# Kernel tuning notes

Hardware: AMD Instinct MI355X
Metric: run time of the kernel (lower is better)

The kernel has to match this reference:

```python
import jax, jax.numpy as jnp
import numpy as np

DT = 0.1       # integration step (ms)
TAU_M = 10.0   # membrane time constant
TAU_S = 5.0    # synaptic time constant
E_REV = 1.0    # synaptic reversal potential
G_MAX = 1.0    # synaptic conductance scale
P, N, E, B, T = 8, 2048, 16, 4, 128


def setup_inputs() -> dict:
    key = jax.random.key(0)
    k_src, k_tgt, k_w, k_win = jax.random.split(key, 4)
    t_seq = jnp.arange(B * T, dtype=jnp.float32).reshape(B, T) * DT  # [B,T] times in ms
    src = jax.random.randint(k_src, (E,), 0, P, dtype=jnp.int32)
    tgt = jax.random.randint(k_tgt, (E,), 0, P, dtype=jnp.int32)
    W = jax.random.normal(k_w, (E, N, N), jnp.float32) * (1.0 / np.sqrt(N))
    W_in = jax.random.normal(k_win, (N, N), jnp.float32) * (1.0 / np.sqrt(N))
    v0 = jnp.zeros((P, B, N), jnp.float32)      # population states
    s0 = jnp.zeros((E, B, N), jnp.float32)      # recurrent synapse states
    s_in0 = jnp.zeros((B, N), jnp.float32)      # input synapse state
    return dict(t_seq=t_seq, W=W, W_in=W_in, v0=v0, s0=s0, s_in0=s_in0, src=src, tgt=tgt)


def _input_rate(t, n):
    # InputPopulation: firing rate is a pure function of time t, per-unit phase.
    phase = jnp.arange(n, dtype=jnp.float32) * (2.0 * jnp.pi / n)
    return 0.5 * (1.0 + jnp.sin(2.0 * jnp.pi * t[:, None] / 100.0 + phase[None, :]))  # [B,n]


def _simulate(t_seq, W, W_in, v0, s0, s_in0, src, tgt):
    n_pop = v0.shape[0]

    def step(carry, t):  # t: [B] current time
        v, s, s_in, err = carry
        rates = jax.nn.sigmoid(v)                      # [P,B,N] firing rates
        # --- synapse message passing: gather pre rates, dense projection ---
        pre = rates[src]                               # [E,B,N]
        drive = jnp.einsum('ebi,eij->ebj', pre, W)     # [E,B,N]
        s_new = s + DT * (-s / TAU_S + drive)          # exponential synapse state
        # --- input population synapse (pre rate is a function of t) ---
        rate_in = _input_rate(t, v.shape[-1])          # [B,N]
        s_in_new = s_in + DT * (-s_in / TAU_S + rate_in @ W_in)
        # --- conductance-based currents scattered into target populations ---
        post_v = v[tgt]                                # [E,B,N]
        I_e = G_MAX * s_new * (E_REV - post_v)
        g_e = G_MAX * s_new
        I_sum = jax.ops.segment_sum(I_e, tgt, num_segments=n_pop)  # [P,B,N]
        g_sum = jax.ops.segment_sum(g_e, tgt, num_segments=n_pop)
        I_in = G_MAX * s_in_new * (E_REV - v[0])
        I_sum = I_sum.at[0].add(I_in)
        g_sum = g_sum.at[0].add(G_MAX * s_in_new)
        # --- Euler integrator step + stability error accumulation ---
        dv = (-v - g_sum * v + I_sum) / TAU_M
        v_new = v + DT * dv
        err_new = err + jnp.mean(jnp.abs(dv)) * DT
        return (v_new, s_new, s_in_new, err_new), jax.nn.sigmoid(v_new)

    init = (v0, s0, s_in0, jnp.zeros((), jnp.float32))
    (v_f, s_f, s_in_f, err), rates_seq = jax.lax.scan(step, init, t_seq.T)  # rates_seq: [T,P,B,N]
    firing_rates = jnp.transpose(rates_seq, (2, 0, 1, 3))  # [B,T,P,N]
    return firing_rates, err


def reference(t_seq, W, W_in, v0, s0, s_in0, src, tgt):
    return _simulate(t_seq, W, W_in, v0, s0, s_in0, src, tgt)
```

## Files before the change

### kernel.cpp

```cpp
#include <hip/hip_runtime.h>
#include <hip/hip_bf16.h>
#include <math.h>

#define DT_     0.1f
#define TAU_M_  10.0f
#define TAU_S_  5.0f
#define NP_     8
#define NN_     2048
#define NE_     16
#define NB_     4
#define NT_     128

#define CH_     32
#define IL_     64
#define NEDGE_  17

typedef __attribute__((ext_vector_type(8))) _Float16 half8;
typedef __attribute__((ext_vector_type(8))) float    float8;

template <typename T> struct V8;
template <> struct V8<float>    { typedef float8 type; };
template <> struct V8<_Float16> { typedef half8  type; };

__device__ __forceinline__ float sigmoidf_(float x) {
  return 1.0f / (1.0f + expf(-x));
}

__global__ __launch_bounds__(256) void k_convert(
    const float* __restrict__ W, const float* __restrict__ W_in,
    _Float16* __restrict__ Wh) {
  size_t idx = ((size_t)blockIdx.x * 256 + threadIdx.x) * 8;
  const size_t lim = (size_t)NE_ * NN_ * NN_;
  const float* src = (idx < lim) ? (W + idx) : (W_in + (idx - lim));
  float4 a = *(const float4*)src;
  float4 b = *(const float4*)(src + 4);
  half8 h;
  h[0] = (_Float16)a.x; h[1] = (_Float16)a.y; h[2] = (_Float16)a.z; h[3] = (_Float16)a.w;
  h[4] = (_Float16)b.x; h[5] = (_Float16)b.y; h[6] = (_Float16)b.z; h[7] = (_Float16)b.w;
  *(half8*)(Wh + idx) = h;
}

__global__ __launch_bounds__(256) void k_init(
    const float* __restrict__ v0, const float* __restrict__ s0,
    const float* __restrict__ s_in0,
    float* __restrict__ v, float* __restrict__ s, float* __restrict__ s_in,
    float* __restrict__ rates, float* __restrict__ errpart) {
  int idx = blockIdx.x * 256 + threadIdx.x;
  if (idx < NE_ * NB_ * NN_) s[idx] = s0[idx];
  if (idx < NP_ * NB_ * NN_) {
    float vv = v0[idx];
    v[idx] = vv;
    rates[idx] = sigmoidf_(vv);
  }
  if (idx < NB_ * NN_) s_in[idx] = s_in0[idx];
  if (idx < 256) errpart[idx] = 0.0f;
}

template <typename WT>
__global__ __launch_bounds__(256) void k_stepA(
    const WT* __restrict__ Wall, const WT* __restrict__ Win,
    const float* __restrict__ rates, const float* __restrict__ t_seq,
    const int* __restrict__ src, _Float16* __restrict__ part, int step) {
  const int e   = blockIdx.x;
  const int ch  = blockIdx.y;
  const int tid = threadIdx.x;

  __shared__ float pre[NB_][IL_];
  const int i0 = ch * IL_;

  if (tid < NB_ * IL_) {
    int b  = tid >> 6;
    int il = tid & (IL_ - 1);
    float val;
    if (e == 16) {
      float t = t_seq[b * NT_ + step];
      float phase = (float)(i0 + il) * (6.2831853071795864f / (float)NN_);
      val = 0.5f * (1.0f + sinf(0.062831853071795864f * t + phase));
    } else {
      val = rates[(src[e] * NB_ + b) * NN_ + (i0 + il)];
    }
    pre[b][il] = val;
  }
  __syncthreads();

  const WT* Wp = (e == 16) ? Win : (Wall + (size_t)e * NN_ * NN_);
  const int j = tid * 8;

  float acc[NB_][8] = {};
  typedef typename V8<WT>::type vec8;
#pragma unroll 8
  for (int il = 0; il < IL_; ++il) {
    vec8 w = *(const vec8*)(Wp + (size_t)(i0 + il) * NN_ + j);
    float wf[8];
#pragma unroll
    for (int k = 0; k < 8; ++k) wf[k] = (float)w[k];
#pragma unroll
    for (int b = 0; b < NB_; ++b) {
      float p = pre[b][il];
#pragma unroll
      for (int k = 0; k < 8; ++k) acc[b][k] += p * wf[k];
    }
  }

#pragma unroll
  for (int b = 0; b < NB_; ++b) {
    half8 o;
#pragma unroll
    for (int k = 0; k < 8; ++k) o[k] = (_Float16)acc[b][k];
    *(half8*)(part + (((size_t)ch * NEDGE_ + e) * NB_ + b) * NN_ + j) = o;
  }
}

__global__ __launch_bounds__(256) void k_stepR(
    const _Float16* __restrict__ part, float* __restrict__ s,
    float* __restrict__ s_in) {
  const int idx = blockIdx.x * 256 + threadIdx.x;
  const int e  = idx >> 10;
  const int r  = idx & 1023;
  const int b  = r >> 8;
  const int n  = (r & 255) * 8;

  float acc[8] = {};
#pragma unroll
  for (int c = 0; c < CH_; ++c) {
    half8 pv = *(const half8*)(part + (((size_t)c * NEDGE_ + e) * NB_ + b) * NN_ + n);
#pragma unroll
    for (int k = 0; k < 8; ++k) acc[k] += (float)pv[k];
  }

  float* sp = (e == 16) ? (s_in + b * NN_ + n) : (s + ((size_t)e * NB_ + b) * NN_ + n);
  float4 s0 = *(const float4*)sp;
  float4 s1 = *(const float4*)(sp + 4);
  s0.x += DT_ * (acc[0] - s0.x * (1.0f / TAU_S_));
  s0.y += DT_ * (acc[1] - s0.y * (1.0f / TAU_S_));
  s0.z += DT_ * (acc[2] - s0.z * (1.0f / TAU_S_));
  s0.w += DT_ * (acc[3] - s0.w * (1.0f / TAU_S_));
  s1.x += DT_ * (acc[4] - s1.x * (1.0f / TAU_S_));
  s1.y += DT_ * (acc[5] - s1.y * (1.0f / TAU_S_));
  s1.z += DT_ * (acc[6] - s1.z * (1.0f / TAU_S_));
  s1.w += DT_ * (acc[7] - s1.w * (1.0f / TAU_S_));
  *(float4*)sp       = s0;
  *(float4*)(sp + 4) = s1;
}

__global__ __launch_bounds__(256) void k_stepB(
    const float* __restrict__ s, const float* __restrict__ s_in,
    const int* __restrict__ tgt,
    float* __restrict__ v, float* __restrict__ rates,
    float* __restrict__ errpart, float* __restrict__ out, int step) {
  const int idx = blockIdx.x * 256 + threadIdx.x;
  const int p = idx >> 13;
  const int b = (idx >> 11) & (NB_ - 1);
  const int n = idx & (NN_ - 1);

  int tg[NE_];
#pragma unroll
  for (int e = 0; e < NE_; ++e) tg[e] = tgt[e];

  float S = 0.0f;
#pragma unroll
  for (int e = 0; e < NE_; ++e) {
    if (tg[e] == p) S += s[((size_t)e * NB_ + b) * NN_ + n];
  }
  if (p == 0) S += s_in[b * NN_ + n];

  float* vp = v + ((size_t)p * NB_ + b) * NN_ + n;
  float vv = *vp;
  float I  = S * (1.0f - vv);
  float dv = (-vv - S * vv + I) * (1.0f / TAU_M_);
  float vn = vv + DT_ * dv;
  *vp = vn;
  float rr = sigmoidf_(vn);
  rates[((size_t)p * NB_ + b) * NN_ + n] = rr;
  __builtin_nontemporal_store(rr, out + (((size_t)b * NT_ + step) * NP_ + p) * NN_ + n);

  __shared__ float red[256];
  red[threadIdx.x] = fabsf(dv);
  __syncthreads();
  for (int w = 128; w > 0; w >>= 1) {
    if (threadIdx.x < w) red[threadIdx.x] += red[threadIdx.x + w];
    __syncthreads();
  }
  if (threadIdx.x == 0) {
    errpart[blockIdx.x] += red[0] * (DT_ / (float)(NP_ * NB_ * NN_));
  }
}

__global__ void k_final(const float* __restrict__ errpart,
                        float* __restrict__ out_err) {
  if (threadIdx.x == 0) {
    float sum = 0.0f;
    for (int i = 0; i < 256; ++i) sum += errpart[i];
    *out_err = sum;
  }
}

extern "C" void kernel_launch(void* const* d_in, const int* in_sizes, int n_in,
                              void* d_out, int out_size, void* d_ws, size_t ws_size,
                              hipStream_t stream) {
  const float* t_seq = (const float*)d_in[0];
  const float* W     = (const float*)d_in[1];
  const float* W_in  = (const float*)d_in[2];
  const float* v0    = (const float*)d_in[3];
  const float* s0    = (const float*)d_in[4];
  const float* s_in0 = (const float*)d_in[5];
  const int*   src   = (const int*)d_in[6];
  const int*   tgt   = (const int*)d_in[7];
  float* out = (float*)d_out;

  const size_t WH_ELEMS = (size_t)NEDGE_ * NN_ * NN_;
  const size_t PART_H   = (size_t)CH_ * NEDGE_ * NB_ * NN_;
  const size_t STATE_F  = 65536 + 131072 + 8192 + 65536 + 256;
  const size_t NEED_H   = (WH_ELEMS + PART_H) * sizeof(_Float16) + STATE_F * sizeof(float);
  const bool useHalf = ws_size >= NEED_H;

  _Float16* Wh;
  _Float16* part;
  if (useHalf) {
    Wh   = (_Float16*)d_ws;
    part = Wh + WH_ELEMS;
  } else {
    Wh   = nullptr;
    part = (_Float16*)d_ws;
  }
  float* v       = (float*)(part + PART_H);
  float* s       = v + NP_ * NB_ * NN_;
  float* s_in    = s + NE_ * NB_ * NN_;
  float* rates   = s_in + NB_ * NN_;
  float* errpart = rates + NP_ * NB_ * NN_;

  if (useHalf) {
    hipLaunchKernelGGL(k_convert, dim3((unsigned)(WH_ELEMS / (8 * 256))), dim3(256),
                       0, stream, W, W_in, Wh);
  }
  hipLaunchKernelGGL(k_init, dim3(512), dim3(256), 0, stream,
                     v0, s0, s_in0, v, s, s_in, rates, errpart);

  for (int t = 0; t < NT_; ++t) {
    if (useHalf) {
      hipLaunchKernelGGL(k_stepA<_Float16>, dim3(NEDGE_, CH_), dim3(256), 0, stream,
                         Wh, Wh + (size_t)NE_ * NN_ * NN_, rates, t_seq, src, part, t);
    } else {
      hipLaunchKernelGGL(k_stepA<float>, dim3(NEDGE_, CH_), dim3(256), 0, stream,
                         W, W_in, rates, t_seq, src, part, t);
    }
    hipLaunchKernelGGL(k_stepR, dim3(68), dim3(256), 0, stream, part, s, s_in);
    hipLaunchKernelGGL(k_stepB, dim3(256), dim3(256), 0, stream,
                       s, s_in, tgt, v, rates, errpart, out, t);
  }

  hipLaunchKernelGGL(k_final, dim3(1), dim3(64), 0, stream,
                     errpart, out + (size_t)NB_ * NT_ * NP_ * NN_);
}
```

Baseline: 4.375 ms.

## Fuse reduce and neuron update kernels, halve the chunk count of the projection

Merges the partial-sum reduction kernel and the membrane update kernel into one kernel. Each block reduces the chunk partials for all 17 edges, updates the synapse state, keeps it in shared memory and then updates all 8 populations. This saves one launch per step and a round trip of the synapse state through global memory. The projection now uses 16 chunks of 128 rows instead of 32 chunks of 64, which halves the partial-sum traffic but also halves the stepA grid. The fused kernel runs only 32 blocks with scalar fp16 loads, so it may be latency-bound with low parallelism.

Result: slower. 4.806 ms (+9.8%).

```diff
diff --git a/kernel.cpp b/kernel.cpp
--- a/kernel.cpp
+++ b/kernel.cpp
@@ -11,8 +11,8 @@
 #define NB_     4
 #define NT_     128
 
-#define CH_     32
-#define IL_     64
+#define CH_     16
+#define IL_     128
 #define NEDGE_  17
 
 typedef __attribute__((ext_vector_type(8))) _Float16 half8;
@@ -53,7 +53,7 @@
     rates[idx] = sigmoidf_(vv);
   }
   if (idx < NB_ * NN_) s_in[idx] = s_in0[idx];
-  if (idx < 256) errpart[idx] = 0.0f;
+  if (idx < 64) errpart[idx] = 0.0f;
 }
 
 template <typename WT>
@@ -68,9 +68,9 @@
   __shared__ float pre[NB_][IL_];
   const int i0 = ch * IL_;
 
-  if (tid < NB_ * IL_) {
-    int b  = tid >> 6;
-    int il = tid & (IL_ - 1);
+  for (int k = tid; k < NB_ * IL_; k += 256) {
+    int b  = k >> 7;
+    int il = k & (IL_ - 1);
     float val;
     if (e == 16) {
       float t = t_seq[b * NT_ + step];
@@ -88,7 +88,7 @@
 
   float acc[NB_][8] = {};
   typedef typename V8<WT>::type vec8;
-#pragma unroll 8
+#pragma unroll 4
   for (int il = 0; il < IL_; ++il) {
     vec8 w = *(const vec8*)(Wp + (size_t)(i0 + il) * NN_ + j);
     float wf[8];
@@ -111,78 +111,67 @@
   }
 }
 
-__global__ __launch_bounds__(256) void k_stepR(
-    const _Float16* __restrict__ part, float* __restrict__ s,
-    float* __restrict__ s_in) {
-  const int idx = blockIdx.x * 256 + threadIdx.x;
-  const int e  = idx >> 10;
-  const int r  = idx & 1023;
-  const int b  = r >> 8;
-  const int n  = (r & 255) * 8;
-
-  float acc[8] = {};
-#pragma unroll
-  for (int c = 0; c < CH_; ++c) {
-    half8 pv = *(const half8*)(part + (((size_t)c * NEDGE_ + e) * NB_ + b) * NN_ + n);
-#pragma unroll
-    for (int k = 0; k < 8; ++k) acc[k] += (float)pv[k];
-  }
-
-  float* sp = (e == 16) ? (s_in + b * NN_ + n) : (s + ((size_t)e * NB_ + b) * NN_ + n);
-  float4 s0 = *(const float4*)sp;
-  float4 s1 = *(const float4*)(sp + 4);
-  s0.x += DT_ * (acc[0] - s0.x * (1.0f / TAU_S_));
-  s0.y += DT_ * (acc[1] - s0.y * (1.0f / TAU_S_));
-  s0.z += DT_ * (acc[2] - s0.z * (1.0f / TAU_S_));
-  s0.w += DT_ * (acc[3] - s0.w * (1.0f / TAU_S_));
-  s1.x += DT_ * (acc[4] - s1.x * (1.0f / TAU_S_));
-  s1.y += DT_ * (acc[5] - s1.y * (1.0f / TAU_S_));
-  s1.z += DT_ * (acc[6] - s1.z * (1.0f / TAU_S_));
-  s1.w += DT_ * (acc[7] - s1.w * (1.0f / TAU_S_));
-  *(float4*)sp       = s0;
-  *(float4*)(sp + 4) = s1;
-}
-
-__global__ __launch_bounds__(256) void k_stepB(
-    const float* __restrict__ s, const float* __restrict__ s_in,
-    const int* __restrict__ tgt,
-    float* __restrict__ v, float* __restrict__ rates,
-    float* __restrict__ errpart, float* __restrict__ out, int step) {
-  const int idx = blockIdx.x * 256 + threadIdx.x;
-  const int p = idx >> 13;
-  const int b = (idx >> 11) & (NB_ - 1);
-  const int n = idx & (NN_ - 1);
+__global__ __launch_bounds__(256) void k_stepRB(
+    const _Float16* __restrict__ part, const int* __restrict__ tgt,
+    float* __restrict__ v, float* __restrict__ s, float* __restrict__ s_in,
+    float* __restrict__ rates, float* __restrict__ errpart,
+    float* __restrict__ out, int step) {
+  const int blk = blockIdx.x;
+  const int b   = blk >> 3;
+  const int n   = (blk & 7) * 256 + threadIdx.x;
+  const int tid = threadIdx.x;
+
+  __shared__ float sh_s[NEDGE_][256];
+
+#pragma unroll
+  for (int e = 0; e < NEDGE_; ++e) {
+    float acc = 0.0f;
+#pragma unroll
+    for (int c = 0; c < CH_; ++c)
+      acc += (float)part[(((size_t)c * NEDGE_ + e) * NB_ + b) * NN_ + n];
+    float* sp = (e == 16) ? (s_in + b * NN_ + n)
+                          : (s + ((size_t)e * NB_ + b) * NN_ + n);
+    float sv = *sp;
+    sv += DT_ * (acc - sv * (1.0f / TAU_S_));
+    *sp = sv;
+    sh_s[e][tid] = sv;
+  }
+  __syncthreads();
 
   int tg[NE_];
 #pragma unroll
   for (int e = 0; e < NE_; ++e) tg[e] = tgt[e];
 
-  float S = 0.0f;
-#pragma unroll
-  for (int e = 0; e < NE_; ++e) {
-    if (tg[e] == p) S += s[((size_t)e * NB_ + b) * NN_ + n];
-  }
-  if (p == 0) S += s_in[b * NN_ + n];
-
-  float* vp = v + ((size_t)p * NB_ + b) * NN_ + n;
-  float vv = *vp;
-  float I  = S * (1.0f - vv);
-  float dv = (-vv - S * vv + I) * (1.0f / TAU_M_);
-  float vn = vv + DT_ * dv;
-  *vp = vn;
-  float rr = sigmoidf_(vn);
-  rates[((size_t)p * NB_ + b) * NN_ + n] = rr;
-  __builtin_nontemporal_store(rr, out + (((size_t)b * NT_ + step) * NP_ + p) * NN_ + n);
+  float errsum = 0.0f;
+#pragma unroll
+  for (int p = 0; p < NP_; ++p) {
+    float S = 0.0f;
+#pragma unroll
+    for (int e = 0; e < NE_; ++e)
+      if (tg[e] == p) S += sh_s[e][tid];
+    if (p == 0) S += sh_s[16][tid];
+
+    float* vp = v + ((size_t)p * NB_ + b) * NN_ + n;
+    float vv = *vp;
+    float I  = S * (1.0f - vv);
+    float dv = (-vv - S * vv + I) * (1.0f / TAU_M_);
+    float vn = vv + DT_ * dv;
+    *vp = vn;
+    errsum += fabsf(dv);
+    float rr = sigmoidf_(vn);
+    rates[((size_t)p * NB_ + b) * NN_ + n] = rr;
+    __builtin_nontemporal_store(rr, out + (((size_t)b * NT_ + step) * NP_ + p) * NN_ + n);
+  }
 
   __shared__ float red[256];
-  red[threadIdx.x] = fabsf(dv);
+  red[tid] = errsum;
   __syncthreads();
   for (int w = 128; w > 0; w >>= 1) {
-    if (threadIdx.x < w) red[threadIdx.x] += red[threadIdx.x + w];
+    if (tid < w) red[tid] += red[tid + w];
     __syncthreads();
   }
-  if (threadIdx.x == 0) {
-    errpart[blockIdx.x] += red[0] * (DT_ / (float)(NP_ * NB_ * NN_));
+  if (tid == 0) {
+    errpart[blk] += red[0] * (DT_ / (float)(NP_ * NB_ * NN_));
   }
 }
 
@@ -190,7 +179,7 @@
                         float* __restrict__ out_err) {
   if (threadIdx.x == 0) {
     float sum = 0.0f;
-    for (int i = 0; i < 256; ++i) sum += errpart[i];
+    for (int i = 0; i < 32; ++i) sum += errpart[i];
     *out_err = sum;
   }
 }
@@ -244,9 +233,8 @@
       hipLaunchKernelGGL(k_stepA<float>, dim3(NEDGE_, CH_), dim3(256), 0, stream,
                          W, W_in, rates, t_seq, src, part, t);
     }
-    hipLaunchKernelGGL(k_stepR, dim3(68), dim3(256), 0, stream, part, s, s_in);
-    hipLaunchKernelGGL(k_stepB, dim3(256), dim3(256), 0, stream,
-                       s, s_in, tgt, v, rates, errpart, out, t);
+    hipLaunchKernelGGL(k_stepRB, dim3(32), dim3(256), 0, stream,
+                       part, tgt, v, s, s_in, rates, errpart, out, t);
   }
 
   hipLaunchKernelGGL(k_final, dim3(1), dim3(64), 0, stream,
```

## Fuse split-K reduction into matvec kernel via shared-memory column-tile reduce

Applied to the files above, without the earlier changes.

The GEMV kernel is restructured so each block owns a 128-column output tile for one edge and splits the 2048-row K dimension across 16 thread groups. The partial sums are reduced in shared memory and the synapse state is updated in place. This removes the separate reduction kernel and the global fp16 partial buffer, saving one launch per step and the partial write/read traffic. The grid shrinks from 544 to 272 blocks, and each block now stages the full 2048-wide pre-rate vector into shared memory. Error-scale multiplication is moved to the final kernel.

Result: slower. 5.034 ms (+15.1%).

```diff
diff --git a/kernel.cpp b/kernel.cpp
--- a/kernel.cpp
+++ b/kernel.cpp
@@ -10,10 +10,12 @@
 #define NE_     16
 #define NB_     4
 #define NT_     128
-
-#define CH_     32
-#define IL_     64
 #define NEDGE_  17
+
+#define JT_     16
+#define JW_     128
+#define ST_     16
+#define RS_     128
 
 typedef __attribute__((ext_vector_type(8))) _Float16 half8;
 typedef __attribute__((ext_vector_type(8))) float    float8;
@@ -57,90 +59,89 @@
 }
 
 template <typename WT>
-__global__ __launch_bounds__(256) void k_stepA(
+__global__ __launch_bounds__(256) void k_stepA2(
     const WT* __restrict__ Wall, const WT* __restrict__ Win,
     const float* __restrict__ rates, const float* __restrict__ t_seq,
-    const int* __restrict__ src, _Float16* __restrict__ part, int step) {
+    const int* __restrict__ src,
+    float* __restrict__ s, float* __restrict__ s_in, int t) {
   const int e   = blockIdx.x;
-  const int ch  = blockIdx.y;
+  const int jt  = blockIdx.y;
   const int tid = threadIdx.x;
 
-  __shared__ float pre[NB_][IL_];
-  const int i0 = ch * IL_;
-
-  if (tid < NB_ * IL_) {
-    int b  = tid >> 6;
-    int il = tid & (IL_ - 1);
-    float val;
-    if (e == 16) {
-      float t = t_seq[b * NT_ + step];
-      float phase = (float)(i0 + il) * (6.2831853071795864f / (float)NN_);
-      val = 0.5f * (1.0f + sinf(0.062831853071795864f * t + phase));
-    } else {
-      val = rates[(src[e] * NB_ + b) * NN_ + (i0 + il)];
-    }
-    pre[b][il] = val;
+  __shared__ float preT[NB_][NN_];
+  __shared__ float redf[ST_][16][33];
+
+  if (e == 16) {
+    for (int k = tid; k < NB_ * NN_; k += 256) {
+      int b = k >> 11, i = k & (NN_ - 1);
+      float tt = t_seq[b * NT_ + t];
+      float ph = (float)i * (6.2831853071795864f / (float)NN_);
+      preT[b][i] = 0.5f * (1.0f + sinf(0.062831853071795864f * tt + ph));
+    }
+  } else {
+    const int sp = src[e];
+    const float* rp = rates + (size_t)sp * NB_ * NN_;
+    for (int k = tid; k < NB_ * NN_; k += 256) {
+      int b = k >> 11, i = k & (NN_ - 1);
+      preT[b][i] = rp[b * NN_ + i];
+    }
   }
   __syncthreads();
 
   const WT* Wp = (e == 16) ? Win : (Wall + (size_t)e * NN_ * NN_);
-  const int j = tid * 8;
+  const int jc = tid & 15;
+  const int st = tid >> 4;
+  const int j0 = jt * JW_ + jc * 8;
+  const int i0 = st * RS_;
 
   float acc[NB_][8] = {};
   typedef typename V8<WT>::type vec8;
+  const WT* wptr = Wp + (size_t)i0 * NN_ + j0;
 #pragma unroll 8
-  for (int il = 0; il < IL_; ++il) {
-    vec8 w = *(const vec8*)(Wp + (size_t)(i0 + il) * NN_ + j);
-    float wf[8];
-#pragma unroll
-    for (int k = 0; k < 8; ++k) wf[k] = (float)w[k];
-#pragma unroll
-    for (int b = 0; b < NB_; ++b) {
-      float p = pre[b][il];
-#pragma unroll
-      for (int k = 0; k < 8; ++k) acc[b][k] += p * wf[k];
-    }
-  }
-
-#pragma unroll
-  for (int b = 0; b < NB_; ++b) {
-    half8 o;
-#pragma unroll
-    for (int k = 0; k < 8; ++k) o[k] = (_Float16)acc[b][k];
-    *(half8*)(part + (((size_t)ch * NEDGE_ + e) * NB_ + b) * NN_ + j) = o;
-  }
-}
-
-__global__ __launch_bounds__(256) void k_stepR(
-    const _Float16* __restrict__ part, float* __restrict__ s,
-    float* __restrict__ s_in) {
-  const int idx = blockIdx.x * 256 + threadIdx.x;
-  const int e  = idx >> 10;
-  const int r  = idx & 1023;
-  const int b  = r >> 8;
-  const int n  = (r & 255) * 8;
-
-  float acc[8] = {};
-#pragma unroll
-  for (int c = 0; c < CH_; ++c) {
-    half8 pv = *(const half8*)(part + (((size_t)c * NEDGE_ + e) * NB_ + b) * NN_ + n);
-#pragma unroll
-    for (int k = 0; k < 8; ++k) acc[k] += (float)pv[k];
-  }
-
-  float* sp = (e == 16) ? (s_in + b * NN_ + n) : (s + ((size_t)e * NB_ + b) * NN_ + n);
-  float4 s0 = *(const float4*)sp;
-  float4 s1 = *(const float4*)(sp + 4);
-  s0.x += DT_ * (acc[0] - s0.x * (1.0f / TAU_S_));
-  s0.y += DT_ * (acc[1] - s0.y * (1.0f / TAU_S_));
-  s0.z += DT_ * (acc[2] - s0.z * (1.0f / TAU_S_));
-  s0.w += DT_ * (acc[3] - s0.w * (1.0f / TAU_S_));
-  s1.x += DT_ * (acc[4] - s1.x * (1.0f / TAU_S_));
-  s1.y += DT_ * (acc[5] - s1.y * (1.0f / TAU_S_));
-  s1.z += DT_ * (acc[6] - s1.z * (1.0f / TAU_S_));
-  s1.w += DT_ * (acc[7] - s1.w * (1.0f / TAU_S_));
-  *(float4*)sp       = s0;
-  *(float4*)(sp + 4) = s1;
+  for (int r = 0; r < RS_; ++r) {
+    vec8 w = *(const vec8*)wptr;
+    wptr += NN_;
+    float p0 = preT[0][i0 + r];
+    float p1 = preT[1][i0 + r];
+    float p2 = preT[2][i0 + r];
+    float p3 = preT[3][i0 + r];
+#pragma unroll
+    for (int k = 0; k < 8; ++k) {
+      float wk = (float)w[k];
+      acc[0][k] += p0 * wk;
+      acc[1][k] += p1 * wk;
+      acc[2][k] += p2 * wk;
+      acc[3][k] += p3 * wk;
+    }
+  }
+
+#pragma unroll
+  for (int b = 0; b < NB_; ++b)
+#pragma unroll
+    for (int k = 0; k < 8; ++k)
+      redf[st][jc][b * 8 + k] = acc[b][k];
+  __syncthreads();
+
+#pragma unroll
+  for (int q = 0; q < 2; ++q) {
+    int slot = tid * 2 + q;
+    int sjc  = slot >> 5;
+    int m    = slot & 31;
+    float d = 0.0f;
+#pragma unroll
+    for (int s2 = 0; s2 < ST_; ++s2) d += redf[s2][sjc][m];
+    int b = m >> 3, k = m & 7;
+    int n = jt * JW_ + sjc * 8 + k;
+    if (e < NE_) {
+      float* sp2 = s + ((size_t)e * NB_ + b) * NN_ + n;
+      float sv = *sp2;
+      *sp2 = sv + DT_ * (d - sv * (1.0f / TAU_S_));
+    } else {
+      float* sp2 = s_in + b * NN_ + n;
+      float sv = *sp2;
+      *sp2 = sv + DT_ * (d - sv * (1.0f / TAU_S_));
+    }
+  }
 }
 
 __global__ __launch_bounds__(256) void k_stepB(
@@ -182,16 +183,16 @@
     __syncthreads();
   }
   if (threadIdx.x == 0) {
-    errpart[blockIdx.x] += red[0] * (DT_ / (float)(NP_ * NB_ * NN_));
-  }
-}
-
-__global__ void k_final(const float* __restrict__ errpart,
-                        float* __restrict__ out_err) {
+    errpart[blockIdx.x] += red[0];
+  }
+}
+
+__global__ void k_err(const float* __restrict__ errpart,
+                      float* __restrict__ out_err) {
   if (threadIdx.x == 0) {
     float sum = 0.0f;
     for (int i = 0; i < 256; ++i) sum += errpart[i];
-    *out_err = sum;
+    *out_err = sum * (DT_ / (float)(NP_ * NB_ * NN_));
   }
 }
 
@@ -209,46 +210,41 @@
   float* out = (float*)d_out;
 
   const size_t WH_ELEMS = (size_t)NEDGE_ * NN_ * NN_;
-  const size_t PART_H   = (size_t)CH_ * NEDGE_ * NB_ * NN_;
-  const size_t STATE_F  = 65536 + 131072 + 8192 + 65536 + 256;
-  const size_t NEED_H   = (WH_ELEMS + PART_H) * sizeof(_Float16) + STATE_F * sizeof(float);
+  const size_t SB = (size_t)NE_ * NB_ * NN_;
+  const size_t VB = (size_t)NP_ * NB_ * NN_;
+  const size_t IB = (size_t)NB_ * NN_;
+  const size_t STATE_F = SB + VB + IB + VB + 256;
+  const size_t NEED_H = WH_ELEMS * sizeof(_Float16) + STATE_F * sizeof(float);
   const bool useHalf = ws_size >= NEED_H;
 
-  _Float16* Wh;
-  _Float16* part;
+  _Float16* Wh = useHalf ? (_Float16*)d_ws : nullptr;
+  float* fbase = useHalf ? (float*)(Wh + WH_ELEMS) : (float*)d_ws;
+  float* s       = fbase;
+  float* v       = s + SB;
+  float* s_in    = v + VB;
+  float* rates   = s_in + IB;
+  float* errpart = rates + VB;
+
   if (useHalf) {
-    Wh   = (_Float16*)d_ws;
-    part = Wh + WH_ELEMS;
-  } else {
-    Wh   = nullptr;
-    part = (_Float16*)d_ws;
-  }
-  float* v       = (float*)(part + PART_H);
-  float* s       = v + NP_ * NB_ * NN_;
-  float* s_in    = s + NE_ * NB_ * NN_;
-  float* rates   = s_in + NB_ * NN_;
-  float* errpart = rates + NP_ * NB_ * NN_;
-
-  if (useHalf) {
-    hipLaunchKernelGGL(k_convert, dim3((unsigned)(WH_ELEMS / (8 * 256))), dim3(256),
-                       0, stream, W, W_in, Wh);
+    hipLaunchKernelGGL(k_convert, dim3((unsigned)(WH_ELEMS / (8 * 256))),
+                       dim3(256), 0, stream, W, W_in, Wh);
   }
   hipLaunchKernelGGL(k_init, dim3(512), dim3(256), 0, stream,
                      v0, s0, s_in0, v, s, s_in, rates, errpart);
 
   for (int t = 0; t < NT_; ++t) {
     if (useHalf) {
-      hipLaunchKernelGGL(k_stepA<_Float16>, dim3(NEDGE_, CH_), dim3(256), 0, stream,
-                         Wh, Wh + (size_t)NE_ * NN_ * NN_, rates, t_seq, src, part, t);
+      hipLaunchKernelGGL((k_stepA2<_Float16>), dim3(NEDGE_, JT_), dim3(256), 0,
+                         stream, Wh, Wh + (size_t)NE_ * NN_ * NN_,
+                         rates, t_seq, src, s, s_in, t);
     } else {
-      hipLaunchKernelGGL(k_stepA<float>, dim3(NEDGE_, CH_), dim3(256), 0, stream,
-                         W, W_in, rates, t_seq, src, part, t);
-    }
-    hipLaunchKernelGGL(k_stepR, dim3(68), dim3(256), 0, stream, part, s, s_in);
+      hipLaunchKernelGGL((k_stepA2<float>), dim3(NEDGE_, JT_), dim3(256), 0,
+                         stream, W, W_in, rates, t_seq, src, s, s_in, t);
+    }
     hipLaunchKernelGGL(k_stepB, dim3(256), dim3(256), 0, stream,
                        s, s_in, tgt, v, rates, errpart, out, t);
   }
 
-  hipLaunchKernelGGL(k_final, dim3(1), dim3(64), 0, stream,
+  hipLaunchKernelGGL(k_err, dim3(1), dim3(64), 0, stream,
                      errpart, out + (size_t)NB_ * NT_ * NP_ * NN_);
 }
```
